# Performance work log

Measured on AMD Instinct MI355X. Metric: run time of the kernel, lower is better.

The kernel has to match this reference:

```python
import jax, jax.numpy as jnp
import numpy as np

N = 20000      # nodes
E = 640000     # edges
FIN = 256
FQK = 256


def setup_inputs() -> dict:
    key = jax.random.key(0)
    kx, ks, kd, kw = jax.random.split(key, 4)
    x = jax.random.normal(kx, (N, FIN), dtype=jnp.float32)
    # src must be sorted (original scatter_softmax assumes grouped index);
    # force last element to N-1 so nbatches == N as in batch[-1]+1.
    src = jnp.sort(jax.random.randint(ks, (E,), 0, N))
    src = src.at[-1].set(N - 1)
    dest = jax.random.randint(kd, (E,), 0, N)
    ei = jnp.stack([src, dest]).astype(jnp.int64)
    # nn.Linear(Fin, 2*Fqk, bias=False) weight: [2*Fqk, Fin]
    bound = 1.0 / np.sqrt(FIN)
    W = jax.random.uniform(kw, (2 * FQK, FIN), dtype=jnp.float32,
                           minval=-bound, maxval=bound)
    return {"x": x, "ei": ei, "W": W}


def reference(x, ei, W):
    src, dest = ei[0], ei[1]
    n_nodes = x.shape[0]
    scaling = FQK ** -0.5
    qk = x @ W.T                      # [N, 2*Fqk]
    q, k = jnp.split(qk, 2, axis=-1)  # each [N, Fqk]
    q = q * scaling
    # per-edge dot product: (q[src] . k[dest])  -> [E]
    aw = jnp.einsum('ef,ef->e', q[src], k[dest])
    # scatter softmax over edges grouped by src node (raw exp, as original)
    ex = jnp.exp(aw)
    expsum = jax.ops.segment_sum(ex, src, num_segments=n_nodes)  # [N]
    return ex / expsum[src]
```

## Files before the change

kernel.cpp:

```cpp
#include <hip/hip_runtime.h>
#include <cmath>

#define FIN 256
#define FQK 256
#define SCALING 0.0625f
#define MAX_SEG 256
#define ASTRIDE 264

typedef __bf16 bf16_t;
typedef bf16_t bf16x8 __attribute__((ext_vector_type(8)));
typedef float  f32x4  __attribute__((ext_vector_type(4)));
typedef float  f32x2  __attribute__((ext_vector_type(2)));

__device__ __forceinline__ unsigned short f2bf(float f) {
    unsigned int u = __float_as_uint(f);
    u += 0x7FFFu + ((u >> 16) & 1u);
    return (unsigned short)(u >> 16);
}
__device__ __forceinline__ float bf_lo(unsigned int w) { return __uint_as_float(w << 16); }
__device__ __forceinline__ float bf_hi(unsigned int w) { return __uint_as_float(w & 0xFFFF0000u); }

__device__ __forceinline__ bf16x8 cvt8(float4 a, float4 b) {
    bf16x8 r;
    r[0] = (bf16_t)a.x; r[1] = (bf16_t)a.y; r[2] = (bf16_t)a.z; r[3] = (bf16_t)a.w;
    r[4] = (bf16_t)b.x; r[5] = (bf16_t)b.y; r[6] = (bf16_t)b.z; r[7] = (bf16_t)b.w;
    return r;
}

__global__ __launch_bounds__(256) void m_seg_kernel(const float* __restrict__ W,
                                                    unsigned short* __restrict__ MbF,
                                                    const int* __restrict__ src,
                                                    int* __restrict__ seg, int N, int E) {
    const int b = blockIdx.x;
    if (b < FIN) {
        const int f = b;
        const int k = threadIdx.x;
        const float* __restrict__ Wq = W;
        const float* __restrict__ Wk = W + FQK * FIN;
        float acc = 0.f;
#pragma unroll 8
        for (int c = 0; c < FQK; ++c)
            acc += Wq[c * FIN + f] * Wk[c * FIN + k];
        const int ft  = f >> 4, m16 = f & 15;
        const int kcI = k >> 5, q = (k >> 3) & 3, e = k & 7;
        MbF[(size_t)(((kcI * 16 + ft) * 64 + q * 16 + m16) * 8 + e)] = f2bf(acc * SCALING);
    } else {
        const int n = (b - FIN) * 256 + threadIdx.x;
        if (n > N) return;
        int lo = 0, hi = E;
        while (lo < hi) {
            const int mid = (lo + hi) >> 1;
            if (src[mid] < n) lo = mid + 1; else hi = mid;
        }
        seg[n] = lo;
    }
}

__global__ __launch_bounds__(256) void gemm_y_kernel(const float* __restrict__ x,
                                                     const unsigned short* __restrict__ MbF,
                                                     unsigned short* __restrict__ y, int N) {
    __shared__ unsigned short sA[32 * ASTRIDE];

    const int t    = threadIdx.x;
    const int wv   = t >> 6;
    const int lane = t & 63;
    const int q    = lane >> 4;
    const int m16  = lane & 15;
    const int n0   = blockIdx.x * 32;
    const int f0   = wv * 64;

    {
        const int rsub = t >> 5;
        const int col  = (t & 31) * 8;
#pragma unroll
        for (int p = 0; p < 4; ++p) {
            const int r  = p * 8 + rsub;
            const int n  = n0 + r;
            const int nc = n < N ? n : N - 1;
            const float* __restrict__ xp = x + (size_t)nc * FIN + col;
            const float4 a = *(const float4*)(xp);
            const float4 b = *(const float4*)(xp + 4);
            *(bf16x8*)&sA[r * ASTRIDE + col] = cvt8(a, b);
        }
    }
    __syncthreads();

    f32x4 acc[2][4] = {};

#pragma unroll
    for (int kc = 0; kc < FIN; kc += 32) {
        bf16x8 afrag[2];
#pragma unroll
        for (int mt = 0; mt < 2; ++mt)
            afrag[mt] = *(const bf16x8*)&sA[(mt * 16 + m16) * ASTRIDE + kc + q * 8];

        const unsigned short* __restrict__ bp =
            MbF + (size_t)(((kc >> 5) * 16 + (f0 >> 4)) * 64 + lane) * 8;
#pragma unroll
        for (int ft = 0; ft < 4; ++ft) {
            union { uint4 u; bf16x8 v; } bu;
            bu.u = *(const uint4*)(bp + ft * 512);
#pragma unroll
            for (int mt = 0; mt < 2; ++mt)
                acc[mt][ft] = __builtin_amdgcn_mfma_f32_16x16x32_bf16(afrag[mt], bu.v,
                                                                     acc[mt][ft], 0, 0, 0);
        }
    }

    __syncthreads();
#pragma unroll
    for (int mt = 0; mt < 2; ++mt)
#pragma unroll
        for (int r = 0; r < 4; ++r)
#pragma unroll
            for (int ft = 0; ft < 4; ++ft)
                sA[(mt * 16 + q * 4 + r) * ASTRIDE + f0 + ft * 16 + m16] =
                    f2bf(acc[mt][ft][r]);
    __syncthreads();

#pragma unroll
    for (int s = 0; s < 4; ++s) {
        const int row = s * 8 + (t >> 5);
        const int c16 = t & 31;
        const int n   = n0 + row;
        if (n < N) {
            const uint4 v = *(const uint4*)&sA[row * ASTRIDE + c16 * 8];
            *(uint4*)(y + (size_t)n * FIN + c16 * 8) = v;
        }
    }
}

__device__ __forceinline__ f32x2 dotp(unsigned int wq, float xl, float xh, f32x2 acc) {
    f32x2 e;  e[0] = bf_lo(wq); e[1] = bf_hi(wq);
    f32x2 xx; xx[0] = xl;       xx[1] = xh;
    return __builtin_elementwise_fma(e, xx, acc);
}
__device__ __forceinline__ f32x2 dot8v(uint4 qv, float4 xa, float4 xb, f32x2 acc) {
    acc = dotp(qv.x, xa.x, xa.y, acc);
    acc = dotp(qv.y, xa.z, xa.w, acc);
    acc = dotp(qv.z, xb.x, xb.y, acc);
    acc = dotp(qv.w, xb.z, xb.w, acc);
    return acc;
}

__global__ __launch_bounds__(256) void node_edge_kernel(const float* __restrict__ x,
                                                        const unsigned short* __restrict__ y,
                                                        const int* __restrict__ dest,
                                                        const int* __restrict__ seg,
                                                        float* __restrict__ out, int N) {
    __shared__ float exlds[4][MAX_SEG];

    const int w    = threadIdx.x >> 6;
    const int lane = threadIdx.x & 63;
    const int n    = blockIdx.x * 4 + w;
    const int g    = lane >> 3;
    const int j    = lane & 7;

    if (n >= N) return;
    const int s0  = seg[n];
    const int cnt = seg[n + 1] - s0;
    if (cnt <= 0) return;

    float4 xf[8];
    {
        const float* __restrict__ xr = x + (size_t)n * FIN + j * 32;
#pragma unroll
        for (int u = 0; u < 8; ++u) xf[u] = *(const float4*)(xr + u * 4);
    }

    float sum = 0.f;

#define DCLAMP(d) ((unsigned)(d) < (unsigned)N ? (d) : 0)

#define GISSUE(B0, B1, B2, B3, d, valid)                                       \
    if (valid) {                                                               \
        const uint4* __restrict__ yr =                                         \
            (const uint4*)(y + (size_t)DCLAMP(d) * FIN) + j * 4;               \
        B0 = yr[0]; B1 = yr[1]; B2 = yr[2]; B3 = yr[3];                        \
    }

#define CONSUME(B0, B1, B2, B3, idx, valid)                                    \
    if (valid) {                                                               \
        f32x2 a2 = {0.f, 0.f};                                                 \
        a2 = dot8v(B0, xf[0], xf[1], a2);                                      \
        a2 = dot8v(B1, xf[2], xf[3], a2);                                      \
        a2 = dot8v(B2, xf[4], xf[5], a2);                                      \
        a2 = dot8v(B3, xf[6], xf[7], a2);                                      \
        float accv = a2[0] + a2[1];                                            \
        accv += __shfl_xor(accv, 1, 64);                                       \
        accv += __shfl_xor(accv, 2, 64);                                       \
        accv += __shfl_xor(accv, 4, 64);                                       \
        const float ex = __expf(accv);                                         \
        sum += ex;                                                             \
        if (j == 0 && (idx) < MAX_SEG) exlds[w][idx] = ex;                     \
    }

    uint4 A0 = {}, A1 = {}, A2 = {}, A3 = {};
    uint4 B0 = {}, B1 = {}, B2 = {}, B3 = {};
    uint4 C0 = {}, C1 = {}, C2 = {}, C3 = {};

    int  iA = g, iB = g + 8, iC = g + 16;
    bool vA = iA < cnt, vB = iB < cnt, vC = iC < cnt;

    {
        const int dA = vA ? dest[s0 + iA] : 0;
        GISSUE(A0, A1, A2, A3, dA, vA);
        const int dB = vB ? dest[s0 + iB] : 0;
        GISSUE(B0, B1, B2, B3, dB, vB);
        const int dC = vC ? dest[s0 + iC] : 0;
        GISSUE(C0, C1, C2, C3, dC, vC);
    }
    int inext = g + 24;
    int dN    = (inext < cnt) ? dest[s0 + inext] : 0;

    const int nit = (cnt + 7) >> 3;
    for (int it = 0; it < nit; it += 3) {
        CONSUME(A0, A1, A2, A3, iA, vA);
        iA = inext; vA = iA < cnt;
        GISSUE(A0, A1, A2, A3, dN, vA);
        inext += 8; dN = (inext < cnt) ? dest[s0 + inext] : 0;
        CONSUME(B0, B1, B2, B3, iB, vB);
        iB = inext; vB = iB < cnt;
        GISSUE(B0, B1, B2, B3, dN, vB);
        inext += 8; dN = (inext < cnt) ? dest[s0 + inext] : 0;
        CONSUME(C0, C1, C2, C3, iC, vC);
        iC = inext; vC = iC < cnt;
        GISSUE(C0, C1, C2, C3, dN, vC);
        inext += 8; dN = (inext < cnt) ? dest[s0 + inext] : 0;
    }

    sum += __shfl_xor(sum, 8, 64);
    sum += __shfl_xor(sum, 16, 64);
    sum += __shfl_xor(sum, 32, 64);
    const float inv = 1.0f / sum;

    const int lim = cnt < MAX_SEG ? cnt : MAX_SEG;
    for (int i = lane; i < lim; i += 64)
        out[s0 + i] = exlds[w][i] * inv;

#undef GISSUE
#undef CONSUME
#undef DCLAMP
}

extern "C" void kernel_launch(void* const* d_in, const int* in_sizes, int n_in,
                              void* d_out, int out_size, void* d_ws, size_t ws_size,
                              hipStream_t stream) {
    const float* x  = (const float*)d_in[0];
    const int*   ei = (const int*)d_in[1];
    const float* W  = (const float*)d_in[2];
    float* out = (float*)d_out;

    const int N = in_sizes[0] / FIN;
    const int E = in_sizes[1] / 2;

    unsigned short* MbF = (unsigned short*)d_ws;
    unsigned short* y   = MbF + (size_t)FIN * FIN;
    int*            seg = (int*)(y + (size_t)N * FIN);

    const int segBlocks = (N + 256) / 256;
    m_seg_kernel<<<FIN + segBlocks, 256, 0, stream>>>(W, MbF, ei, seg, N, E);

    gemm_y_kernel<<<(N + 31) / 32, 256, 0, stream>>>(x, MbF, y, N);

    node_edge_kernel<<<(N + 3) / 4, 256, 0, stream>>>(x, y, ei + E, seg, out, N);
}
```

Baseline: 140.8 us.

## Switch to fp16 with dot2 edge math, persistent edge kernel, smaller GEMM tiles

Replaces bf16 with fp16 for the M matrix, y and a new half-precision copy of x written by the GEMM kernel. The edge kernel now reads the fp16 x row and uses packed fdot2 instructions instead of unpacking bf16 into fp32 FMAs. It also becomes a grid-stride persistent kernel with 1024 blocks and double rather than triple buffering of gathers. The GEMM tile shrinks to 16 rows per block. The aims are to halve x traffic and ALU work per edge and to cut launch imbalance, at the cost of an extra xh write, fp16 range/precision risk, and less prefetch depth.

```diff
diff --git a/kernel.cpp b/kernel.cpp
--- a/kernel.cpp
+++ b/kernel.cpp
@@ -7,28 +7,37 @@
 #define MAX_SEG 256
 #define ASTRIDE 264
 
-typedef __bf16 bf16_t;
-typedef bf16_t bf16x8 __attribute__((ext_vector_type(8)));
-typedef float  f32x4  __attribute__((ext_vector_type(4)));
-typedef float  f32x2  __attribute__((ext_vector_type(2)));
-
-__device__ __forceinline__ unsigned short f2bf(float f) {
-    unsigned int u = __float_as_uint(f);
-    u += 0x7FFFu + ((u >> 16) & 1u);
-    return (unsigned short)(u >> 16);
-}
-__device__ __forceinline__ float bf_lo(unsigned int w) { return __uint_as_float(w << 16); }
-__device__ __forceinline__ float bf_hi(unsigned int w) { return __uint_as_float(w & 0xFFFF0000u); }
-
-__device__ __forceinline__ bf16x8 cvt8(float4 a, float4 b) {
-    bf16x8 r;
-    r[0] = (bf16_t)a.x; r[1] = (bf16_t)a.y; r[2] = (bf16_t)a.z; r[3] = (bf16_t)a.w;
-    r[4] = (bf16_t)b.x; r[5] = (bf16_t)b.y; r[6] = (bf16_t)b.z; r[7] = (bf16_t)b.w;
+typedef _Float16 f16_t;
+typedef f16_t f16x8 __attribute__((ext_vector_type(8)));
+typedef f16_t f16x2 __attribute__((ext_vector_type(2)));
+typedef float f32x4 __attribute__((ext_vector_type(4)));
+
+__device__ __forceinline__ f16x8 cvt8h(float4 a, float4 b) {
+    f16x8 r;
+    r[0] = (f16_t)a.x; r[1] = (f16_t)a.y; r[2] = (f16_t)a.z; r[3] = (f16_t)a.w;
+    r[4] = (f16_t)b.x; r[5] = (f16_t)b.y; r[6] = (f16_t)b.z; r[7] = (f16_t)b.w;
     return r;
 }
 
+__device__ __forceinline__ float fdot2f(f16x2 a, f16x2 b, float c) {
+#if __has_builtin(__builtin_amdgcn_fdot2)
+    return __builtin_amdgcn_fdot2(a, b, c, false);
+#else
+    return c + (float)a[0] * (float)b[0] + (float)a[1] * (float)b[1];
+#endif
+}
+
+union H16 { uint4 u; f16x2 h[4]; };
+__device__ __forceinline__ float dot16(uint4 ya, uint4 xa, float acc) {
+    H16 A; A.u = ya;
+    H16 X; X.u = xa;
+#pragma unroll
+    for (int i = 0; i < 4; ++i) acc = fdot2f(A.h[i], X.h[i], acc);
+    return acc;
+}
+
 __global__ __launch_bounds__(256) void m_seg_kernel(const float* __restrict__ W,
-                                                    unsigned short* __restrict__ MbF,
+                                                    f16_t* __restrict__ MbF,
                                                     const int* __restrict__ src,
                                                     int* __restrict__ seg, int N, int E) {
     const int b = blockIdx.x;
@@ -43,7 +52,8 @@
             acc += Wq[c * FIN + f] * Wk[c * FIN + k];
         const int ft  = f >> 4, m16 = f & 15;
         const int kcI = k >> 5, q = (k >> 3) & 3, e = k & 7;
-        MbF[(size_t)(((kcI * 16 + ft) * 64 + q * 16 + m16) * 8 + e)] = f2bf(acc * SCALING);
+        MbF[(size_t)(((kcI * 16 + ft) * 64 + q * 16 + m16) * 8 + e)] =
+            (f16_t)(acc * SCALING);
     } else {
         const int n = (b - FIN) * 256 + threadIdx.x;
         if (n > N) return;
@@ -57,186 +67,147 @@
 }
 
 __global__ __launch_bounds__(256) void gemm_y_kernel(const float* __restrict__ x,
-                                                     const unsigned short* __restrict__ MbF,
-                                                     unsigned short* __restrict__ y, int N) {
-    __shared__ unsigned short sA[32 * ASTRIDE];
+                                                     const f16_t* __restrict__ MbF,
+                                                     f16_t* __restrict__ y,
+                                                     f16_t* __restrict__ xh, int N) {
+    __shared__ f16_t sA[16 * ASTRIDE];
 
     const int t    = threadIdx.x;
     const int wv   = t >> 6;
     const int lane = t & 63;
     const int q    = lane >> 4;
     const int m16  = lane & 15;
-    const int n0   = blockIdx.x * 32;
+    const int n0   = blockIdx.x * 16;
     const int f0   = wv * 64;
 
     {
         const int rsub = t >> 5;
         const int col  = (t & 31) * 8;
 #pragma unroll
-        for (int p = 0; p < 4; ++p) {
+        for (int p = 0; p < 2; ++p) {
             const int r  = p * 8 + rsub;
             const int n  = n0 + r;
             const int nc = n < N ? n : N - 1;
             const float* __restrict__ xp = x + (size_t)nc * FIN + col;
             const float4 a = *(const float4*)(xp);
             const float4 b = *(const float4*)(xp + 4);
-            *(bf16x8*)&sA[r * ASTRIDE + col] = cvt8(a, b);
+            const f16x8 v = cvt8h(a, b);
+            *(f16x8*)&sA[r * ASTRIDE + col] = v;
+            if (n < N) *(f16x8*)(xh + (size_t)n * FIN + col) = v;
         }
     }
     __syncthreads();
 
-    f32x4 acc[2][4] = {};
+    f32x4 acc[4] = {};
 
 #pragma unroll
     for (int kc = 0; kc < FIN; kc += 32) {
-        bf16x8 afrag[2];
-#pragma unroll
-        for (int mt = 0; mt < 2; ++mt)
-            afrag[mt] = *(const bf16x8*)&sA[(mt * 16 + m16) * ASTRIDE + kc + q * 8];
-
-        const unsigned short* __restrict__ bp =
+        const f16x8 af = *(const f16x8*)&sA[m16 * ASTRIDE + kc + q * 8];
+        const f16_t* __restrict__ bp =
             MbF + (size_t)(((kc >> 5) * 16 + (f0 >> 4)) * 64 + lane) * 8;
 #pragma unroll
         for (int ft = 0; ft < 4; ++ft) {
-            union { uint4 u; bf16x8 v; } bu;
+            union { uint4 u; f16x8 v; } bu;
             bu.u = *(const uint4*)(bp + ft * 512);
-#pragma unroll
-            for (int mt = 0; mt < 2; ++mt)
-                acc[mt][ft] = __builtin_amdgcn_mfma_f32_16x16x32_bf16(afrag[mt], bu.v,
-                                                                     acc[mt][ft], 0, 0, 0);
+            acc[ft] = __builtin_amdgcn_mfma_f32_16x16x32_f16(af, bu.v, acc[ft], 0, 0, 0);
         }
     }
 
     __syncthreads();
 #pragma unroll
-    for (int mt = 0; mt < 2; ++mt)
+    for (int ft = 0; ft < 4; ++ft)
 #pragma unroll
         for (int r = 0; r < 4; ++r)
-#pragma unroll
-            for (int ft = 0; ft < 4; ++ft)
-                sA[(mt * 16 + q * 4 + r) * ASTRIDE + f0 + ft * 16 + m16] =
-                    f2bf(acc[mt][ft][r]);
+            sA[(q * 4 + r) * ASTRIDE + f0 + ft * 16 + m16] = (f16_t)acc[ft][r];
     __syncthreads();
 
-#pragma unroll
-    for (int s = 0; s < 4; ++s) {
-        const int row = s * 8 + (t >> 5);
-        const int c16 = t & 31;
+    {
+        const int row = t >> 4;
+        const int c   = (t & 15) * 16;
         const int n   = n0 + row;
         if (n < N) {
-            const uint4 v = *(const uint4*)&sA[row * ASTRIDE + c16 * 8];
-            *(uint4*)(y + (size_t)n * FIN + c16 * 8) = v;
-        }
-    }
-}
-
-__device__ __forceinline__ f32x2 dotp(unsigned int wq, float xl, float xh, f32x2 acc) {
-    f32x2 e;  e[0] = bf_lo(wq); e[1] = bf_hi(wq);
-    f32x2 xx; xx[0] = xl;       xx[1] = xh;
-    return __builtin_elementwise_fma(e, xx, acc);
-}
-__device__ __forceinline__ f32x2 dot8v(uint4 qv, float4 xa, float4 xb, f32x2 acc) {
-    acc = dotp(qv.x, xa.x, xa.y, acc);
-    acc = dotp(qv.y, xa.z, xa.w, acc);
-    acc = dotp(qv.z, xb.x, xb.y, acc);
-    acc = dotp(qv.w, xb.z, xb.w, acc);
-    return acc;
-}
-
-__global__ __launch_bounds__(256) void node_edge_kernel(const float* __restrict__ x,
-                                                        const unsigned short* __restrict__ y,
+            const uint4 v0 = *(const uint4*)&sA[row * ASTRIDE + c];
+            const uint4 v1 = *(const uint4*)&sA[row * ASTRIDE + c + 8];
+            *(uint4*)(y + (size_t)n * FIN + c)     = v0;
+            *(uint4*)(y + (size_t)n * FIN + c + 8) = v1;
+        }
+    }
+}
+
+__global__ __launch_bounds__(256) void node_edge_kernel(const f16_t* __restrict__ xh,
+                                                        const f16_t* __restrict__ y,
                                                         const int* __restrict__ dest,
                                                         const int* __restrict__ seg,
-                                                        float* __restrict__ out, int N) {
+                                                        float* __restrict__ out,
+                                                        int N, int E, int nwaves) {
     __shared__ float exlds[4][MAX_SEG];
 
     const int w    = threadIdx.x >> 6;
     const int lane = threadIdx.x & 63;
-    const int n    = blockIdx.x * 4 + w;
     const int g    = lane >> 3;
     const int j    = lane & 7;
 
-    if (n >= N) return;
-    const int s0  = seg[n];
-    const int cnt = seg[n + 1] - s0;
-    if (cnt <= 0) return;
-
-    float4 xf[8];
-    {
-        const float* __restrict__ xr = x + (size_t)n * FIN + j * 32;
-#pragma unroll
-        for (int u = 0; u < 8; ++u) xf[u] = *(const float4*)(xr + u * 4);
-    }
-
-    float sum = 0.f;
-
 #define DCLAMP(d) ((unsigned)(d) < (unsigned)N ? (d) : 0)
 
-#define GISSUE(B0, B1, B2, B3, d, valid)                                       \
+#define GISSUE(B0, B1, B2, B3, i, valid)                                       \
     if (valid) {                                                               \
-        const uint4* __restrict__ yr =                                         \
-            (const uint4*)(y + (size_t)DCLAMP(d) * FIN) + j * 4;               \
+        const int d_ = DCLAMP(dest[s0 + (i)]);                                 \
+        const uint4* __restrict__ yr = (const uint4*)(y + (size_t)d_ * FIN) + j * 4; \
         B0 = yr[0]; B1 = yr[1]; B2 = yr[2]; B3 = yr[3];                        \
     }
 
 #define CONSUME(B0, B1, B2, B3, idx, valid)                                    \
     if (valid) {                                                               \
-        f32x2 a2 = {0.f, 0.f};                                                 \
-        a2 = dot8v(B0, xf[0], xf[1], a2);                                      \
-        a2 = dot8v(B1, xf[2], xf[3], a2);                                      \
-        a2 = dot8v(B2, xf[4], xf[5], a2);                                      \
-        a2 = dot8v(B3, xf[6], xf[7], a2);                                      \
-        float accv = a2[0] + a2[1];                                            \
-        accv += __shfl_xor(accv, 1, 64);                                       \
-        accv += __shfl_xor(accv, 2, 64);                                       \
-        accv += __shfl_xor(accv, 4, 64);                                       \
-        const float ex = __expf(accv);                                         \
+        float a_ = 0.f;                                                        \
+        a_ = dot16(B0, X0, a_);                                                \
+        a_ = dot16(B1, X1, a_);                                                \
+        a_ = dot16(B2, X2, a_);                                                \
+        a_ = dot16(B3, X3, a_);                                                \
+        a_ += __shfl_xor(a_, 1, 64);                                           \
+        a_ += __shfl_xor(a_, 2, 64);                                           \
+        a_ += __shfl_xor(a_, 4, 64);                                           \
+        const float ex = __expf(a_);                                           \
         sum += ex;                                                             \
         if (j == 0 && (idx) < MAX_SEG) exlds[w][idx] = ex;                     \
     }
 
-    uint4 A0 = {}, A1 = {}, A2 = {}, A3 = {};
-    uint4 B0 = {}, B1 = {}, B2 = {}, B3 = {};
-    uint4 C0 = {}, C1 = {}, C2 = {}, C3 = {};
-
-    int  iA = g, iB = g + 8, iC = g + 16;
-    bool vA = iA < cnt, vB = iB < cnt, vC = iC < cnt;
-
-    {
-        const int dA = vA ? dest[s0 + iA] : 0;
-        GISSUE(A0, A1, A2, A3, dA, vA);
-        const int dB = vB ? dest[s0 + iB] : 0;
-        GISSUE(B0, B1, B2, B3, dB, vB);
-        const int dC = vC ? dest[s0 + iC] : 0;
-        GISSUE(C0, C1, C2, C3, dC, vC);
-    }
-    int inext = g + 24;
-    int dN    = (inext < cnt) ? dest[s0 + inext] : 0;
-
-    const int nit = (cnt + 7) >> 3;
-    for (int it = 0; it < nit; it += 3) {
-        CONSUME(A0, A1, A2, A3, iA, vA);
-        iA = inext; vA = iA < cnt;
-        GISSUE(A0, A1, A2, A3, dN, vA);
-        inext += 8; dN = (inext < cnt) ? dest[s0 + inext] : 0;
-        CONSUME(B0, B1, B2, B3, iB, vB);
-        iB = inext; vB = iB < cnt;
-        GISSUE(B0, B1, B2, B3, dN, vB);
-        inext += 8; dN = (inext < cnt) ? dest[s0 + inext] : 0;
-        CONSUME(C0, C1, C2, C3, iC, vC);
-        iC = inext; vC = iC < cnt;
-        GISSUE(C0, C1, C2, C3, dN, vC);
-        inext += 8; dN = (inext < cnt) ? dest[s0 + inext] : 0;
-    }
-
-    sum += __shfl_xor(sum, 8, 64);
-    sum += __shfl_xor(sum, 16, 64);
-    sum += __shfl_xor(sum, 32, 64);
-    const float inv = 1.0f / sum;
-
-    const int lim = cnt < MAX_SEG ? cnt : MAX_SEG;
-    for (int i = lane; i < lim; i += 64)
-        out[s0 + i] = exlds[w][i] * inv;
+    for (int n = blockIdx.x * 4 + w; n < N; n += nwaves) {
+        int s0 = seg[n], s1 = seg[n + 1];
+        s0 = min(max(s0, 0), E);
+        s1 = min(max(s1, 0), E);
+        const int cnt = s1 - s0;
+        if (cnt <= 0) continue;
+
+        const uint4* __restrict__ xp = (const uint4*)(xh + (size_t)n * FIN + j * 32);
+        const uint4 X0 = xp[0], X1 = xp[1], X2 = xp[2], X3 = xp[3];
+
+        float sum = 0.f;
+        const int nit = (cnt + 7) >> 3;
+
+        uint4 A0, A1, A2, A3, B0, B1, B2, B3;
+        bool vA = g < cnt;
+        GISSUE(A0, A1, A2, A3, g, vA);
+
+        for (int it = 0; it < nit; it += 2) {
+            const int iB = (it + 1) * 8 + g;
+            const bool vB = iB < cnt;
+            GISSUE(B0, B1, B2, B3, iB, vB);
+            CONSUME(A0, A1, A2, A3, it * 8 + g, vA);
+            const int iA = (it + 2) * 8 + g;
+            vA = iA < cnt;
+            GISSUE(A0, A1, A2, A3, iA, vA);
+            CONSUME(B0, B1, B2, B3, iB, vB);
+        }
+
+        sum += __shfl_xor(sum, 8, 64);
+        sum += __shfl_xor(sum, 16, 64);
+        sum += __shfl_xor(sum, 32, 64);
+        const float inv = 1.0f / sum;
+
+        const int lim = cnt < MAX_SEG ? cnt : MAX_SEG;
+        for (int i = lane; i < lim; i += 64)
+            out[s0 + i] = exlds[w][i] * inv;
+    }
 
 #undef GISSUE
 #undef CONSUME
@@ -254,14 +225,17 @@
     const int N = in_sizes[0] / FIN;
     const int E = in_sizes[1] / 2;
 
-    unsigned short* MbF = (unsigned short*)d_ws;
-    unsigned short* y   = MbF + (size_t)FIN * FIN;
-    int*            seg = (int*)(y + (size_t)N * FIN);
+    f16_t* MbF = (f16_t*)d_ws;
+    f16_t* y   = MbF + (size_t)FIN * FIN;
+    f16_t* xh  = y + (size_t)N * FIN;
+    int*   seg = (int*)(xh + (size_t)N * FIN);
 
     const int segBlocks = (N + 256) / 256;
     m_seg_kernel<<<FIN + segBlocks, 256, 0, stream>>>(W, MbF, ei, seg, N, E);
 
-    gemm_y_kernel<<<(N + 31) / 32, 256, 0, stream>>>(x, MbF, y, N);
-
-    node_edge_kernel<<<(N + 3) / 4, 256, 0, stream>>>(x, y, ei + E, seg, out, N);
-}
+    gemm_y_kernel<<<(N + 15) / 16, 256, 0, stream>>>(x, MbF, y, xh, N);
+
+    const int neBlocks = 1024;
+    node_edge_kernel<<<neBlocks, 256, 0, stream>>>(xh, y, ei + E, seg, out,
+                                                   N, E, neBlocks * 4);
+}
```

Result: faster. 132.8 us (-5.7%).
